# Optimization experiments

Measured on AMD Instinct MI355X. Metric: run time of the kernel, lower is better.

The kernel has to match this reference:

```python
import jax, jax.numpy as jnp
import numpy as np

EPS = 1e-07

def setup_inputs() -> dict:
    key = jax.random.key(0)
    foreground = jax.random.normal(key, (8, 256, 64, 64), dtype=jnp.float32)
    return {"foreground": foreground}

def reference(foreground):
    bs, ch, h, w = foreground.shape
    # kernels: one 1x1 kernel per spatial position, L2-normalized over channels
    K = foreground.reshape(bs, ch, h * w).transpose(0, 2, 1) + EPS      # [b, hw, c]
    K = K / jnp.sqrt(jnp.sum(K * K, axis=2, keepdims=True))
    # conv2d with 1x1 kernels == per-pixel dot product against every kernel.
    # (padding=patch_size//2 in the torch code is exactly cancelled by the
    #  matching padding of the conv_transpose2d, so it is omitted.)
    scores = jnp.einsum('bkc,bchw->bkhw', K, foreground)                # [b, hw, h, w]
    attn = jax.nn.softmax(scores, axis=1)
    # conv_transpose2d with the same 1x1 kernels == K^T @ attn per pixel
    out = jnp.einsum('bkc,bkhw->bchw', K, attn)                         # [b, c, h, w]
    return out
```

## Files before the change

### kernel.cpp

```cpp
#include <hip/hip_runtime.h>
#include <hip/hip_fp8.h>


#define BATCH 8
#define CH 256
#define NPIX 4096
#define EPSV 1e-7f
#define L2E 1.4426950408889634f

using bf16x8 = __attribute__((ext_vector_type(8))) __bf16;
using bf16x4 = __attribute__((ext_vector_type(4))) __bf16;
using f32x4  = __attribute__((ext_vector_type(4))) float;

__device__ __forceinline__ void gload16(const void* g, void* l) {
  __builtin_amdgcn_global_load_lds(
      (const __attribute__((address_space(1))) unsigned int*)g,
      (__attribute__((address_space(3))) unsigned int*)l, 16, 0, 0);
}

__device__ __forceinline__ void barrier_full() {
  asm volatile("s_waitcnt vmcnt(0) lgkmcnt(0)\n"
               "s_barrier" ::: "memory");
}
__device__ __forceinline__ void barrier_lgkm() {
  asm volatile("s_waitcnt lgkmcnt(0)\n"
               "s_barrier" ::: "memory");
}

__device__ __forceinline__ unsigned char to_fp8(float f) {
  return __hip_cvt_float_to_fp8(f, __HIP_SATFINITE, __HIP_E4M3);
}

__global__ __launch_bounds__(256)
void ca_prep(const float* __restrict__ F, unsigned char* __restrict__ KA,
             __bf16* __restrict__ KB) {
  const int b   = blockIdx.x;
  const int kt  = blockIdx.y;
  const int kt0 = kt * 32;
  const int t   = threadIdx.x;
  const int k   = t & 31;
  const int h   = (t >> 5) & 1;
  const int w   = t >> 6;

  const float* __restrict__ Fb = F + (size_t)b * CH * NPIX;

  __shared__ float red[4][32];
  __shared__ float invk[32];
  __shared__ __align__(16) __bf16 T[32][264];

  float fv[32];
  float ss = 0.f;
#pragma unroll
  for (int rep = 0; rep < 32; ++rep) {
    int c = rep * 8 + w * 2 + h;
    float v = Fb[(size_t)c * NPIX + kt0 + k] + EPSV;
    fv[rep] = v;
    ss = fmaf(v, v, ss);
  }
  ss += __shfl_xor(ss, 32, 64);
  if ((t & 32) == 0) red[w][k] = ss;
  __syncthreads();
  if (t < 32) invk[t] = rsqrtf(red[0][t] + red[1][t] + red[2][t] + red[3][t]);
  __syncthreads();
  const float iv = invk[k];
#pragma unroll
  for (int rep = 0; rep < 32; ++rep) {
    int c = rep * 8 + w * 2 + h;
    T[k][c] = (__bf16)(fv[rep] * iv);
  }
  __syncthreads();

  {
    char* KAp = (char*)KA + ((size_t)b * 128 + kt) * (32 * 256);
#pragma unroll
    for (int pass = 0; pass < 4; ++pass) {
      int slot = pass * 256 + t;
      int krow = slot >> 5;
      int u    = slot & 31;
      bf16x8 v = *(const bf16x8*)&T[krow][u * 8];
      unsigned char pk[8];
#pragma unroll
      for (int j = 0; j < 8; ++j) pk[j] = to_fp8((float)v[j]);
      *(long*)(KAp + krow * 256 + ((u ^ (krow & 15)) * 8)) = *(const long*)pk;
    }
  }
  {
    __bf16* KBp = KB + ((size_t)b * 128 + kt) * (256 * 32);
#pragma unroll
    for (int pass = 0; pass < 4; ++pass) {
      int c = pass * 64 + (t >> 2);
      int v = t & 3;
      bf16x8 o;
#pragma unroll
      for (int j = 0; j < 8; ++j) o[j] = T[v * 8 + j][c];
      *(bf16x8*)&KBp[c * 32 + v * 8] = o;
    }
  }
}

__global__ __launch_bounds__(1024, 4)
void ca_attn12(const float* __restrict__ F, const unsigned char* __restrict__ KA,
               const __bf16* __restrict__ KB, float* __restrict__ Out) {
  __shared__ __align__(16) char smem[65536];

  const int tid  = threadIdx.x;
  const int lane = tid & 63;
  const int w    = tid >> 6;
  const int lq   = lane & 15;
  const int lg   = lane >> 4;
  const int b    = blockIdx.x;
  const int q0   = blockIdx.y * 128;

  const char* KAb = (const char*)KA + (size_t)b * (size_t)NPIX * CH;
  const char* KBb = (const char*)KB + (size_t)b * (size_t)NPIX * CH * 2;
  char* PlB = smem + 32768;

  if (w < 8) {
    const int kh = w >> 2, qh = w & 3;
    const int qA = q0 + qh * 32 + lq;
    const int qB = qA + 16;
    const float* __restrict__ Fb = F + (size_t)b * CH * NPIX;
    const int wo = w * 2048;

#pragma unroll
    for (int j = 0; j < 2; ++j)
      gload16(KAb + wo + j * 1024 + lane * 16, smem + wo + j * 1024);

    long qpA[8], qpB[8];
    float ssA = 0.f, ssB = 0.f;
#pragma unroll
    for (int cf = 0; cf < 8; ++cf) {
      unsigned char pa[8], pb8[8];
#pragma unroll
      for (int j = 0; j < 8; ++j) {
        int c = cf * 32 + lg * 8 + j;
        float va = Fb[(size_t)c * NPIX + qA];
        float vb = Fb[(size_t)c * NPIX + qB];
        pa[j]  = to_fp8(va * L2E);
        pb8[j] = to_fp8(vb * L2E);
        ssA = fmaf(va, va, ssA);
        ssB = fmaf(vb, vb, ssB);
      }
      qpA[cf] = *(const long*)pa;
      qpB[cf] = *(const long*)pb8;
    }
    ssA += __shfl_xor(ssA, 16, 64); ssA += __shfl_xor(ssA, 32, 64);
    ssB += __shfl_xor(ssB, 16, 64); ssB += __shfl_xor(ssB, 32, 64);
    const float mqA = sqrtf(ssA) * L2E, mqB = sqrtf(ssB) * L2E;

    float lA = 0.f, lB = 0.f;
    const int krow = kh * 16 + lq;
    const int rowByte = krow * 256;
    const int ksw = lq & 7;
    const int pwRowA = (qh * 32 + lq) * 128;
    const int pwRowB = pwRowA + 16 * 128;
    const int puBase = kh * 2 + (lg >> 1);
    const int pwSub  = ((lg & 1) << 3);
    const int u0 = (puBase ^ ksw) << 4;
    const int u1 = ((4 + puBase) ^ ksw) << 4;

    barrier_full();

    const f32x4 zero = {0.f, 0.f, 0.f, 0.f};
    for (int i = 0; i < 64; ++i) {
      const int cb = i & 1;
      if (i < 63) {
        const char* s = KAb + (size_t)(i + 1) * 16384;
        char* d = smem + (cb ^ 1) * 16384;
#pragma unroll
        for (int j = 0; j < 2; ++j)
          gload16(s + wo + j * 1024 + lane * 16, d + wo + j * 1024);
      }

      const char* ab0 = smem + cb * 16384 + rowByte;
      const char* ab1 = ab0 + 8192;
      f32x4 s00 = zero, s01 = zero, s10 = zero, s11 = zero;
      __builtin_amdgcn_s_setprio(1);
#pragma unroll
      for (int cf = 0; cf < 8; ++cf) {
        const int uo = ((((cf << 2) | lg) ^ lq) << 3);
        long a0 = *(const long*)(ab0 + uo);
        long a1 = *(const long*)(ab1 + uo);
        s00 = __builtin_amdgcn_mfma_f32_16x16x32_fp8_fp8(a0, qpA[cf], s00, 0, 0, 0);
        s01 = __builtin_amdgcn_mfma_f32_16x16x32_fp8_fp8(a0, qpB[cf], s01, 0, 0, 0);
        s10 = __builtin_amdgcn_mfma_f32_16x16x32_fp8_fp8(a1, qpA[cf], s10, 0, 0, 0);
        s11 = __builtin_amdgcn_mfma_f32_16x16x32_fp8_fp8(a1, qpB[cf], s11, 0, 0, 0);
      }
      __builtin_amdgcn_s_setprio(0);

      char* pb = PlB + cb * 16384;
      bf16x4 pv00, pv01, pv10, pv11;
#pragma unroll
      for (int r = 0; r < 4; ++r) {
        float p00 = __builtin_amdgcn_exp2f(s00[r] - mqA);
        float p01 = __builtin_amdgcn_exp2f(s01[r] - mqB);
        float p10 = __builtin_amdgcn_exp2f(s10[r] - mqA);
        float p11 = __builtin_amdgcn_exp2f(s11[r] - mqB);
        lA += p00 + p10; lB += p01 + p11;
        pv00[r] = (__bf16)p00; pv01[r] = (__bf16)p01;
        pv10[r] = (__bf16)p10; pv11[r] = (__bf16)p11;
      }
      *(bf16x4*)(pb + pwRowA + u0 + pwSub) = pv00;
      *(bf16x4*)(pb + pwRowB + u0 + pwSub) = pv01;
      *(bf16x4*)(pb + pwRowA + u1 + pwSub) = pv10;
      *(bf16x4*)(pb + pwRowB + u1 + pwSub) = pv11;

      barrier_full();
    }

    lA += __shfl_xor(lA, 16, 64); lA += __shfl_xor(lA, 32, 64);
    lB += __shfl_xor(lB, 16, 64); lB += __shfl_xor(lB, 32, 64);
    float* lE = (float*)smem;
    if (lg == 0) lE[kh * 128 + qh * 32 + lq] = lA;
    if (lg == 1) lE[kh * 128 + qh * 32 + 16 + lq] = lB;
    barrier_full();

  } else {
    const int cq  = w - 8;
    const int c0  = (cq >> 1) * 64;
    const int qh2 = cq & 1;
    const size_t fragBase = (size_t)(c0 + lq) * 64 + (size_t)lg * 16;
    const int prRow = (qh2 * 64 + lq) * 128;
    const int prU0  = ((0 * 4 + lg) ^ (lq & 7)) << 4;
    const int prU1  = ((1 * 4 + lg) ^ (lq & 7)) << 4;

    const f32x4 zero = {0.f, 0.f, 0.f, 0.f};
    f32x4 oacc[4][4];
#pragma unroll
    for (int i = 0; i < 4; ++i)
#pragma unroll
      for (int j = 0; j < 4; ++j) oacc[i][j] = zero;

    barrier_lgkm();

    for (int jt = 0; jt < 64; ++jt) {
      const char* kb0 = KBb + (size_t)(2 * jt) * 16384 + fragBase;
      const char* kb1 = kb0 + 16384;
      bf16x8 k00 = *(const bf16x8*)(kb0);
      bf16x8 k01 = *(const bf16x8*)(kb0 + 1024);
      bf16x8 k02 = *(const bf16x8*)(kb0 + 2048);
      bf16x8 k03 = *(const bf16x8*)(kb0 + 3072);
      bf16x8 k10 = *(const bf16x8*)(kb1);
      bf16x8 k11 = *(const bf16x8*)(kb1 + 1024);
      bf16x8 k12 = *(const bf16x8*)(kb1 + 2048);
      bf16x8 k13 = *(const bf16x8*)(kb1 + 3072);

      barrier_lgkm();

      const char* pb = PlB + (jt & 1) * 16384;
      __builtin_amdgcn_s_setprio(1);
#pragma unroll
      for (int qf = 0; qf < 4; ++qf) {
        bf16x8 pf0 = *(const bf16x8*)(pb + prRow + qf * 2048 + prU0);
        oacc[0][qf] = __builtin_amdgcn_mfma_f32_16x16x32_bf16(k00, pf0, oacc[0][qf], 0, 0, 0);
        oacc[1][qf] = __builtin_amdgcn_mfma_f32_16x16x32_bf16(k01, pf0, oacc[1][qf], 0, 0, 0);
        oacc[2][qf] = __builtin_amdgcn_mfma_f32_16x16x32_bf16(k02, pf0, oacc[2][qf], 0, 0, 0);
        oacc[3][qf] = __builtin_amdgcn_mfma_f32_16x16x32_bf16(k03, pf0, oacc[3][qf], 0, 0, 0);
      }
#pragma unroll
      for (int qf = 0; qf < 4; ++qf) {
        bf16x8 pf1 = *(const bf16x8*)(pb + prRow + qf * 2048 + prU1);
        oacc[0][qf] = __builtin_amdgcn_mfma_f32_16x16x32_bf16(k10, pf1, oacc[0][qf], 0, 0, 0);
        oacc[1][qf] = __builtin_amdgcn_mfma_f32_16x16x32_bf16(k11, pf1, oacc[1][qf], 0, 0, 0);
        oacc[2][qf] = __builtin_amdgcn_mfma_f32_16x16x32_bf16(k12, pf1, oacc[2][qf], 0, 0, 0);
        oacc[3][qf] = __builtin_amdgcn_mfma_f32_16x16x32_bf16(k13, pf1, oacc[3][qf], 0, 0, 0);
      }
      __builtin_amdgcn_s_setprio(0);
    }

    barrier_lgkm();

    const float* lE = (const float*)smem;
    const int qb = qh2 * 64;
    float rl0 = 1.0f / (lE[qb + 0 * 16 + lq] + lE[128 + qb + 0 * 16 + lq]);
    float rl1 = 1.0f / (lE[qb + 1 * 16 + lq] + lE[128 + qb + 1 * 16 + lq]);
    float rl2 = 1.0f / (lE[qb + 2 * 16 + lq] + lE[128 + qb + 2 * 16 + lq]);
    float rl3 = 1.0f / (lE[qb + 3 * 16 + lq] + lE[128 + qb + 3 * 16 + lq]);
    float* __restrict__ Ob = Out + (size_t)b * CH * NPIX;
#pragma unroll
    for (int ct = 0; ct < 4; ++ct) {
#pragma unroll
      for (int r = 0; r < 4; ++r) {
        const int c = c0 + ct * 16 + lg * 4 + r;
        float* orow = Ob + (size_t)c * NPIX + q0 + qb;
        orow[0 * 16 + lq] = oacc[ct][0][r] * rl0;
        orow[1 * 16 + lq] = oacc[ct][1][r] * rl1;
        orow[2 * 16 + lq] = oacc[ct][2][r] * rl2;
        orow[3 * 16 + lq] = oacc[ct][3][r] * rl3;
      }
    }
  }
}

extern "C" void kernel_launch(void* const* d_in, const int* in_sizes, int n_in,
                              void* d_out, int out_size, void* d_ws, size_t ws_size,
                              hipStream_t stream) {
  const float* F = (const float*)d_in[0];
  float* out = (float*)d_out;
  const size_t imgBytes = (size_t)BATCH * NPIX * CH;

  unsigned char* KAi = (unsigned char*)d_ws;
  __bf16* KBi = (__bf16*)((char*)d_ws + imgBytes);
  ca_prep<<<dim3(BATCH, 128), 256, 0, stream>>>(F, KAi, KBi);
  ca_attn12<<<dim3(BATCH, 32), 1024, 0, stream>>>(F, KAi, KBi, out);
}
```

Before: 127.7 us.

## Double key tile per iteration to halve barriers and prefetch KB fragments

After: 124.9 us. 2.2% less time.

```diff
diff --git a/kernel.cpp b/kernel.cpp
--- a/kernel.cpp
+++ b/kernel.cpp
@@ -99,9 +99,9 @@
 }
 
 __global__ __launch_bounds__(1024, 4)
-void ca_attn12(const float* __restrict__ F, const unsigned char* __restrict__ KA,
+void ca_attn13(const float* __restrict__ F, const unsigned char* __restrict__ KA,
                const __bf16* __restrict__ KB, float* __restrict__ Out) {
-  __shared__ __align__(16) char smem[65536];
+  __shared__ __align__(16) char smem[131072];
 
   const int tid  = threadIdx.x;
   const int lane = tid & 63;
@@ -113,17 +113,17 @@
 
   const char* KAb = (const char*)KA + (size_t)b * (size_t)NPIX * CH;
   const char* KBb = (const char*)KB + (size_t)b * (size_t)NPIX * CH * 2;
-  char* PlB = smem + 32768;
+  char* PlB = smem + 65536;
 
   if (w < 8) {
     const int kh = w >> 2, qh = w & 3;
     const int qA = q0 + qh * 32 + lq;
     const int qB = qA + 16;
     const float* __restrict__ Fb = F + (size_t)b * CH * NPIX;
-    const int wo = w * 2048;
-
-#pragma unroll
-    for (int j = 0; j < 2; ++j)
+    const int wo = w * 4096;
+
+#pragma unroll
+    for (int j = 0; j < 4; ++j)
       gload16(KAb + wo + j * 1024 + lane * 16, smem + wo + j * 1024);
 
     long qpA[8], qpB[8];
@@ -149,61 +149,59 @@
     const float mqA = sqrtf(ssA) * L2E, mqB = sqrtf(ssB) * L2E;
 
     float lA = 0.f, lB = 0.f;
-    const int krow = kh * 16 + lq;
-    const int rowByte = krow * 256;
     const int ksw = lq & 7;
-    const int pwRowA = (qh * 32 + lq) * 128;
-    const int pwRowB = pwRowA + 16 * 128;
-    const int puBase = kh * 2 + (lg >> 1);
+    const int pwRowA = (qh * 32 + lq) * 256;
+    const int pwRowB = pwRowA + 16 * 256;
     const int pwSub  = ((lg & 1) << 3);
-    const int u0 = (puBase ^ ksw) << 4;
-    const int u1 = ((4 + puBase) ^ ksw) << 4;
+    const int puBase = kh * 8 + (lg >> 1);
 
     barrier_full();
 
     const f32x4 zero = {0.f, 0.f, 0.f, 0.f};
-    for (int i = 0; i < 64; ++i) {
+    for (int i = 0; i < 32; ++i) {
       const int cb = i & 1;
-      if (i < 63) {
-        const char* s = KAb + (size_t)(i + 1) * 16384;
-        char* d = smem + (cb ^ 1) * 16384;
-#pragma unroll
-        for (int j = 0; j < 2; ++j)
+      if (i < 31) {
+        const char* s = KAb + (size_t)(i + 1) * 32768;
+        char* d = smem + (cb ^ 1) * 32768;
+#pragma unroll
+        for (int j = 0; j < 4; ++j)
           gload16(s + wo + j * 1024 + lane * 16, d + wo + j * 1024);
       }
 
-      const char* ab0 = smem + cb * 16384 + rowByte;
-      const char* ab1 = ab0 + 8192;
-      f32x4 s00 = zero, s01 = zero, s10 = zero, s11 = zero;
+      f32x4 acc[4][2];
+#pragma unroll
+      for (int ks = 0; ks < 4; ++ks) { acc[ks][0] = zero; acc[ks][1] = zero; }
+      const char* tb = smem + cb * 32768 + kh * 16384;
       __builtin_amdgcn_s_setprio(1);
 #pragma unroll
       for (int cf = 0; cf < 8; ++cf) {
         const int uo = ((((cf << 2) | lg) ^ lq) << 3);
-        long a0 = *(const long*)(ab0 + uo);
-        long a1 = *(const long*)(ab1 + uo);
-        s00 = __builtin_amdgcn_mfma_f32_16x16x32_fp8_fp8(a0, qpA[cf], s00, 0, 0, 0);
-        s01 = __builtin_amdgcn_mfma_f32_16x16x32_fp8_fp8(a0, qpB[cf], s01, 0, 0, 0);
-        s10 = __builtin_amdgcn_mfma_f32_16x16x32_fp8_fp8(a1, qpA[cf], s10, 0, 0, 0);
-        s11 = __builtin_amdgcn_mfma_f32_16x16x32_fp8_fp8(a1, qpB[cf], s11, 0, 0, 0);
+#pragma unroll
+        for (int ks = 0; ks < 4; ++ks) {
+          const char* ap = tb + (ks >> 1) * 8192 + ((ks & 1) * 16 + lq) * 256 + uo;
+          long a = *(const long*)ap;
+          acc[ks][0] = __builtin_amdgcn_mfma_f32_16x16x32_fp8_fp8(a, qpA[cf], acc[ks][0], 0, 0, 0);
+          acc[ks][1] = __builtin_amdgcn_mfma_f32_16x16x32_fp8_fp8(a, qpB[cf], acc[ks][1], 0, 0, 0);
+        }
       }
       __builtin_amdgcn_s_setprio(0);
 
-      char* pb = PlB + cb * 16384;
-      bf16x4 pv00, pv01, pv10, pv11;
-#pragma unroll
-      for (int r = 0; r < 4; ++r) {
-        float p00 = __builtin_amdgcn_exp2f(s00[r] - mqA);
-        float p01 = __builtin_amdgcn_exp2f(s01[r] - mqB);
-        float p10 = __builtin_amdgcn_exp2f(s10[r] - mqA);
-        float p11 = __builtin_amdgcn_exp2f(s11[r] - mqB);
-        lA += p00 + p10; lB += p01 + p11;
-        pv00[r] = (__bf16)p00; pv01[r] = (__bf16)p01;
-        pv10[r] = (__bf16)p10; pv11[r] = (__bf16)p11;
-      }
-      *(bf16x4*)(pb + pwRowA + u0 + pwSub) = pv00;
-      *(bf16x4*)(pb + pwRowB + u0 + pwSub) = pv01;
-      *(bf16x4*)(pb + pwRowA + u1 + pwSub) = pv10;
-      *(bf16x4*)(pb + pwRowB + u1 + pwSub) = pv11;
+      char* pb = PlB + cb * 32768;
+#pragma unroll
+      for (int ks = 0; ks < 4; ++ks) {
+        bf16x4 pv0, pv1;
+#pragma unroll
+        for (int r = 0; r < 4; ++r) {
+          float p0 = __builtin_amdgcn_exp2f(acc[ks][0][r] - mqA);
+          float p1 = __builtin_amdgcn_exp2f(acc[ks][1][r] - mqB);
+          lA += p0; lB += p1;
+          pv0[r] = (__bf16)p0;
+          pv1[r] = (__bf16)p1;
+        }
+        const int uo = (((puBase + ks * 2) ^ ksw) << 4) + pwSub;
+        *(bf16x4*)(pb + pwRowA + uo) = pv0;
+        *(bf16x4*)(pb + pwRowB + uo) = pv1;
+      }
 
       barrier_full();
     }
@@ -220,9 +218,8 @@
     const int c0  = (cq >> 1) * 64;
     const int qh2 = cq & 1;
     const size_t fragBase = (size_t)(c0 + lq) * 64 + (size_t)lg * 16;
-    const int prRow = (qh2 * 64 + lq) * 128;
-    const int prU0  = ((0 * 4 + lg) ^ (lq & 7)) << 4;
-    const int prU1  = ((1 * 4 + lg) ^ (lq & 7)) << 4;
+    const int prRow = (qh2 * 64 + lq) * 256;
+    const int q7 = lq & 7;
 
     const f32x4 zero = {0.f, 0.f, 0.f, 0.f};
     f32x4 oacc[4][4];
@@ -231,42 +228,59 @@
 #pragma unroll
       for (int j = 0; j < 4; ++j) oacc[i][j] = zero;
 
+    bf16x8 k00, k01, k02, k03, k10, k11, k12, k13;
+
+#define LOADPAIR(JT, KC)                                                      \
+  do {                                                                        \
+    const char* base = KBb + ((size_t)(JT) * 4 + (KC)) * 16384 + fragBase;    \
+    k00 = *(const bf16x8*)(base);                                             \
+    k01 = *(const bf16x8*)(base + 1024);                                      \
+    k02 = *(const bf16x8*)(base + 2048);                                      \
+    k03 = *(const bf16x8*)(base + 3072);                                      \
+    k10 = *(const bf16x8*)(base + 16384);                                     \
+    k11 = *(const bf16x8*)(base + 16384 + 1024);                              \
+    k12 = *(const bf16x8*)(base + 16384 + 2048);                              \
+    k13 = *(const bf16x8*)(base + 16384 + 3072);                              \
+  } while (0)
+
+#define MFMAPAIR(PB, KC)                                                      \
+  do {                                                                        \
+    const char* pb_ = (PB);                                                   \
+    const int u0 = ((((KC) << 2) | lg) ^ q7) << 4;                            \
+    const int u1 = (((((KC) + 1) << 2) | lg) ^ q7) << 4;                      \
+    __builtin_amdgcn_s_setprio(1);                                            \
+    _Pragma("unroll")                                                         \
+    for (int qf = 0; qf < 4; ++qf) {                                          \
+      bf16x8 pf = *(const bf16x8*)(pb_ + prRow + qf * 4096 + u0);             \
+      oacc[0][qf] = __builtin_amdgcn_mfma_f32_16x16x32_bf16(k00, pf, oacc[0][qf], 0, 0, 0); \
+      oacc[1][qf] = __builtin_amdgcn_mfma_f32_16x16x32_bf16(k01, pf, oacc[1][qf], 0, 0, 0); \
+      oacc[2][qf] = __builtin_amdgcn_mfma_f32_16x16x32_bf16(k02, pf, oacc[2][qf], 0, 0, 0); \
+      oacc[3][qf] = __builtin_amdgcn_mfma_f32_16x16x32_bf16(k03, pf, oacc[3][qf], 0, 0, 0); \
+    }                                                                         \
+    _Pragma("unroll")                                                         \
+    for (int qf = 0; qf < 4; ++qf) {                                          \
+      bf16x8 pf = *(const bf16x8*)(pb_ + prRow + qf * 4096 + u1);             \
+      oacc[0][qf] = __builtin_amdgcn_mfma_f32_16x16x32_bf16(k10, pf, oacc[0][qf], 0, 0, 0); \
+      oacc[1][qf] = __builtin_amdgcn_mfma_f32_16x16x32_bf16(k11, pf, oacc[1][qf], 0, 0, 0); \
+      oacc[2][qf] = __builtin_amdgcn_mfma_f32_16x16x32_bf16(k12, pf, oacc[2][qf], 0, 0, 0); \
+      oacc[3][qf] = __builtin_amdgcn_mfma_f32_16x16x32_bf16(k13, pf, oacc[3][qf], 0, 0, 0); \
+    }                                                                         \
+    __builtin_amdgcn_s_setprio(0);                                            \
+  } while (0)
+
     barrier_lgkm();
-
-    for (int jt = 0; jt < 64; ++jt) {
-      const char* kb0 = KBb + (size_t)(2 * jt) * 16384 + fragBase;
-      const char* kb1 = kb0 + 16384;
-      bf16x8 k00 = *(const bf16x8*)(kb0);
-      bf16x8 k01 = *(const bf16x8*)(kb0 + 1024);
-      bf16x8 k02 = *(const bf16x8*)(kb0 + 2048);
-      bf16x8 k03 = *(const bf16x8*)(kb0 + 3072);
-      bf16x8 k10 = *(const bf16x8*)(kb1);
-      bf16x8 k11 = *(const bf16x8*)(kb1 + 1024);
-      bf16x8 k12 = *(const bf16x8*)(kb1 + 2048);
-      bf16x8 k13 = *(const bf16x8*)(kb1 + 3072);
-
+    LOADPAIR(0, 0);
+
+    for (int jt = 0; jt < 32; ++jt) {
       barrier_lgkm();
-
-      const char* pb = PlB + (jt & 1) * 16384;
-      __builtin_amdgcn_s_setprio(1);
-#pragma unroll
-      for (int qf = 0; qf < 4; ++qf) {
-        bf16x8 pf0 = *(const bf16x8*)(pb + prRow + qf * 2048 + prU0);
-        oacc[0][qf] = __builtin_amdgcn_mfma_f32_16x16x32_bf16(k00, pf0, oacc[0][qf], 0, 0, 0);
-        oacc[1][qf] = __builtin_amdgcn_mfma_f32_16x16x32_bf16(k01, pf0, oacc[1][qf], 0, 0, 0);
-        oacc[2][qf] = __builtin_amdgcn_mfma_f32_16x16x32_bf16(k02, pf0, oacc[2][qf], 0, 0, 0);
-        oacc[3][qf] = __builtin_amdgcn_mfma_f32_16x16x32_bf16(k03, pf0, oacc[3][qf], 0, 0, 0);
-      }
-#pragma unroll
-      for (int qf = 0; qf < 4; ++qf) {
-        bf16x8 pf1 = *(const bf16x8*)(pb + prRow + qf * 2048 + prU1);
-        oacc[0][qf] = __builtin_amdgcn_mfma_f32_16x16x32_bf16(k10, pf1, oacc[0][qf], 0, 0, 0);
-        oacc[1][qf] = __builtin_amdgcn_mfma_f32_16x16x32_bf16(k11, pf1, oacc[1][qf], 0, 0, 0);
-        oacc[2][qf] = __builtin_amdgcn_mfma_f32_16x16x32_bf16(k12, pf1, oacc[2][qf], 0, 0, 0);
-        oacc[3][qf] = __builtin_amdgcn_mfma_f32_16x16x32_bf16(k13, pf1, oacc[3][qf], 0, 0, 0);
-      }
-      __builtin_amdgcn_s_setprio(0);
-    }
+      const char* pb = PlB + (jt & 1) * 32768;
+      MFMAPAIR(pb, 0);
+      LOADPAIR(jt, 2);
+      MFMAPAIR(pb, 2);
+      if (jt < 31) LOADPAIR(jt + 1, 0);
+    }
+#undef LOADPAIR
+#undef MFMAPAIR
 
     barrier_lgkm();
 
@@ -302,5 +316,5 @@
   unsigned char* KAi = (unsigned char*)d_ws;
   __bf16* KBi = (__bf16*)((char*)d_ws + imgBytes);
   ca_prep<<<dim3(BATCH, 128), 256, 0, stream>>>(F, KAi, KBi);
-  ca_attn12<<<dim3(BATCH, 32), 1024, 0, stream>>>(F, KAi, KBi, out);
-}
+  ca_attn13<<<dim3(BATCH, 32), 1024, 0, stream>>>(F, KAi, KBi, out);
+}
```
